# Kernel tuning notes

Measured on AMD Instinct MI355X. Metric: run time of the kernel, lower is better.

Reference implementation:

```python
import jax, jax.numpy as jnp
import numpy as np

B, T, LA, L = 4, 32, 32, 512
D, H, C = 2048, 16, 128
KV_DIM = 2048
K = T * LA  # total kv tokens per batch element
EPS = 1e-5


def _ln(x):
    m = jnp.mean(x, axis=-1, keepdims=True)
    v = jnp.var(x, axis=-1, keepdims=True)
    return (x - m) * jax.lax.rsqrt(v + EPS)


def setup_inputs() -> dict:
    key = jax.random.key(0)
    ks = jax.random.split(key, 10)
    s = 1.0 / np.sqrt(D)
    sk = 1.0 / np.sqrt(KV_DIM)
    return {
        "x": jax.random.normal(ks[0], (B, T, LA, KV_DIM), jnp.float32),
        "latents": jax.random.normal(ks[1], (B, L, D), jnp.float32),
        "t_emb": jax.random.normal(ks[2], (B, 3, D), jnp.float32) * 0.02,
        "q_lens": jnp.full((B,), L, dtype=jnp.int32),
        "k_lens": jax.random.randint(ks[3], (B,), K // 2, K + 1).astype(jnp.int32),
        "ln_kv_w": jnp.ones((KV_DIM,), jnp.float32),
        "ln_kv_b": jnp.zeros((KV_DIM,), jnp.float32),
        "ssg": jax.random.normal(ks[4], (1, 3, D), jnp.float32) * s,  # shift_scale_gate param (adaLN=True)
        "Wq": jax.random.normal(ks[5], (D, D), jnp.float32) * s,
        "bq": jnp.zeros((D,), jnp.float32),
        "Wkv": jax.random.normal(ks[6], (KV_DIM, 2 * D), jnp.float32) * sk,
        "bkv": jnp.zeros((2 * D,), jnp.float32),
        "Wo": jax.random.normal(ks[7], (D, D), jnp.float32) * s,
        "bo": jnp.zeros((D,), jnp.float32),
    }


def reference(x, latents, t_emb, q_lens, k_lens, ln_kv_w, ln_kv_b, ssg,
              Wq, bq, Wkv, bkv, Wo, bo):
    # norm_kv (affine LayerNorm over kv_dim)
    xk = _ln(x) * ln_kv_w + ln_kv_b  # (B,T,LA,KV_DIM)
    # AdaLN modulate: shift/scale/gate from t_emb + learned shift_scale_gate
    mod = t_emb + ssg  # (B,3,D)
    shift, scale, gate = mod[:, 0:1], mod[:, 1:2], mod[:, 2:3]  # (B,1,D)
    norm_q = _ln(latents)  # norm_q has no affine when adaLN=True
    lat = norm_q * (1.0 + scale) + shift
    # projections
    q = (lat @ Wq + bq).reshape(B, L, H, C)
    kv = (xk.reshape(B, K, KV_DIM) @ Wkv + bkv)  # (B,K,2D)
    k, v = kv[..., :D], kv[..., D:]
    k = k.reshape(B, K, H, C)
    v = v.reshape(B, K, H, C)
    # varlen attention == per-batch masked attention (keys beyond k_lens masked)
    scores = jnp.einsum("blhc,bkhc->bhlk", q, k) / np.sqrt(C)
    kmask = jnp.arange(K)[None, :] < k_lens[:, None]  # (B,K)
    scores = jnp.where(kmask[:, None, None, :], scores, jnp.finfo(scores.dtype).min)
    attn = jax.nn.softmax(scores, axis=-1)
    out = jnp.einsum("bhlk,bkhc->blhc", attn, v).reshape(B, L, D)
    # queries beyond q_lens are invalid -> zero them (varlen packing semantics)
    qmask = (jnp.arange(L)[None, :] < q_lens[:, None])[..., None]  # (B,L,1)
    out = out * qmask
    return (out @ Wo + bo) * gate
```

## Files before the change

### kernel.cpp

```cpp
#include <hip/hip_runtime.h>

typedef unsigned short u16;
typedef short bf16x8 __attribute__((ext_vector_type(8)));
typedef float f32x4 __attribute__((ext_vector_type(4)));

#define MFMA_BF16(a, b, c) __builtin_amdgcn_mfma_f32_16x16x32_bf16((a), (b), (c), 0, 0, 0)
#define ATT_SCALE 0.08838834764831845f

__device__ __forceinline__ u16 f2bf(float f) {
  union { float f; unsigned int u; } cv;
  cv.f = f;
  unsigned int u = cv.u + 0x7fffu + ((cv.u >> 16) & 1u);
  return (u16)(u >> 16);
}

__global__ __launch_bounds__(256) void ln_fused_kernel(
    const float* __restrict__ x, const float* __restrict__ w,
    const float* __restrict__ b, const float* __restrict__ latents,
    const float* __restrict__ t_emb, const float* __restrict__ ssg,
    u16* __restrict__ xk_out, u16* __restrict__ lat_out)
{
  const int blk = blockIdx.x;
  const bool is_x = blk < 4096;
  const int row = is_x ? blk : blk - 4096;
  const int tid = threadIdx.x;
  const float* src = is_x ? (x + (size_t)row * 2048) : (latents + (size_t)row * 2048);
  const float4* xr = (const float4*)src;
  float4 v0 = xr[tid];
  float4 v1 = xr[tid + 256];
  float sum = v0.x + v0.y + v0.z + v0.w + v1.x + v1.y + v1.z + v1.w;
  float sq  = v0.x*v0.x + v0.y*v0.y + v0.z*v0.z + v0.w*v0.w
            + v1.x*v1.x + v1.y*v1.y + v1.z*v1.z + v1.w*v1.w;
  #pragma unroll
  for (int off = 32; off > 0; off >>= 1) {
    sum += __shfl_xor(sum, off);
    sq  += __shfl_xor(sq, off);
  }
  __shared__ float red[8];
  if ((tid & 63) == 0) { red[tid >> 6] = sum; red[(tid >> 6) + 4] = sq; }
  __syncthreads();
  sum = red[0] + red[1] + red[2] + red[3];
  sq  = red[4] + red[5] + red[6] + red[7];
  const float mean = sum * (1.0f / 2048.0f);
  const float var  = sq * (1.0f / 2048.0f) - mean * mean;
  const float rstd = rsqrtf(var + 1e-5f);
  if (is_x) {
    const float4* w4 = (const float4*)w;
    const float4* b4 = (const float4*)b;
    ushort4* orow = (ushort4*)(xk_out + (size_t)row * 2048);
    #pragma unroll
    for (int j = 0; j < 2; ++j) {
      const int idx = tid + j * 256;
      const float4 v = j ? v1 : v0;
      const float4 ww = w4[idx];
      const float4 bb = b4[idx];
      ushort4 o;
      o.x = f2bf((v.x - mean) * rstd * ww.x + bb.x);
      o.y = f2bf((v.y - mean) * rstd * ww.y + bb.y);
      o.z = f2bf((v.z - mean) * rstd * ww.z + bb.z);
      o.w = f2bf((v.w - mean) * rstd * ww.w + bb.w);
      orow[idx] = o;
    }
  } else {
    const int bidx = row >> 9;
    const float4* te = (const float4*)(t_emb + (size_t)bidx * 3 * 2048);
    const float4* sg = (const float4*)ssg;
    ushort4* orow = (ushort4*)(lat_out + (size_t)row * 2048);
    #pragma unroll
    for (int j = 0; j < 2; ++j) {
      const int idx = tid + j * 256;
      const float4 v = j ? v1 : v0;
      const float4 t0 = te[idx];
      const float4 t1 = te[512 + idx];
      const float4 s0 = sg[idx];
      const float4 s1 = sg[512 + idx];
      ushort4 o;
      o.x = f2bf(((v.x - mean) * rstd) * (1.0f + t1.x + s1.x) + (t0.x + s0.x));
      o.y = f2bf(((v.y - mean) * rstd) * (1.0f + t1.y + s1.y) + (t0.y + s0.y));
      o.z = f2bf(((v.z - mean) * rstd) * (1.0f + t1.z + s1.z) + (t0.z + s0.z));
      o.w = f2bf(((v.w - mean) * rstd) * (1.0f + t1.w + s1.w) + (t0.w + s0.w));
      orow[idx] = o;
    }
  }
}

__global__ __launch_bounds__(256) void transpose_all_kernel(
    const float* __restrict__ Wq, const float* __restrict__ Wo,
    const float* __restrict__ Wkv,
    u16* __restrict__ WqT, u16* __restrict__ WoT, u16* __restrict__ WkvT)
{
  __shared__ float tile[32][33];
  int t = blockIdx.x;
  const float* in;
  u16* outp;
  int C, cx, ry;
  if (t < 4096)       { in = Wq;  outp = WqT;  C = 2048; cx = t & 63;  ry = t >> 6; }
  else if (t < 8192)  { t -= 4096; in = Wo;  outp = WoT;  C = 2048; cx = t & 63;  ry = t >> 6; }
  else                { t -= 8192; in = Wkv; outp = WkvT; C = 4096; cx = t & 127; ry = t >> 7; }
  const int R = 2048;
  const int c0 = cx * 32;
  const int r0 = ry * 32;
  const int tx = threadIdx.x & 31;
  const int ty = threadIdx.x >> 5;
  #pragma unroll
  for (int i = 0; i < 4; ++i)
    tile[ty + i * 8][tx] = in[(size_t)(r0 + ty + i * 8) * C + c0 + tx];
  __syncthreads();
  #pragma unroll
  for (int i = 0; i < 4; ++i)
    outp[(size_t)(c0 + ty + i * 8) * R + r0 + tx] = f2bf(tile[tx][ty + i * 8]);
}

template<int BM, int MODE>
__global__ __launch_bounds__(256) void gemm_bf16_kernel(
    const u16* __restrict__ A, const u16* __restrict__ BT,
    int Kd,
    const float* __restrict__ bias,
    u16* __restrict__ out_q, u16* __restrict__ out_k, u16* __restrict__ out_vT,
    float* __restrict__ out_f,
    const float* __restrict__ t_emb, const float* __restrict__ ssg)
{
  constexpr int TI = BM / 32;
  __shared__ u16 As[2][BM][40];
  __shared__ u16 Bs[2][128][40];
  const int tid  = threadIdx.x;
  const int lane = tid & 63;
  const int wv   = tid >> 6;
  const int wm   = wv & 1, wn = wv >> 1;
  const int quad = lane >> 4, lq = lane & 15;
  const int m0 = blockIdx.y * BM, n0 = blockIdx.x * 128;

  f32x4 acc[TI][4];
  #pragma unroll
  for (int i = 0; i < TI; ++i)
    #pragma unroll
    for (int j = 0; j < 4; ++j)
      acc[i][j] = (f32x4){0.f, 0.f, 0.f, 0.f};

  const int rB  = tid >> 1;
  const int hfB = (tid & 1) * 16;
  const u16* gB = BT + (size_t)(n0 + rB) * Kd + hfB;
  const int rA  = (BM == 128) ? (tid >> 1) : (tid >> 2);
  const int hA  = (BM == 128) ? 0 : ((tid >> 1) & 1);
  const int hfA = (tid & 1) * 16;
  const u16* gA = A + (size_t)(m0 + rA) * Kd + hA * 32 + hfA;

  for (int k0 = 0; k0 < Kd; k0 += 64) {
    uint4 a00, a01, a10, a11;
    a00 = *(const uint4*)(gA + k0);
    a01 = *(const uint4*)(gA + k0 + 8);
    if (BM == 128) {
      a10 = *(const uint4*)(gA + k0 + 32);
      a11 = *(const uint4*)(gA + k0 + 40);
    }
    const uint4 b00 = *(const uint4*)(gB + k0);
    const uint4 b01 = *(const uint4*)(gB + k0 + 8);
    const uint4 b10 = *(const uint4*)(gB + k0 + 32);
    const uint4 b11 = *(const uint4*)(gB + k0 + 40);
    __syncthreads();
    *(uint4*)&As[hA][rA][hfA]     = a00;
    *(uint4*)&As[hA][rA][hfA + 8] = a01;
    if (BM == 128) {
      *(uint4*)&As[1][rA][hfA]     = a10;
      *(uint4*)&As[1][rA][hfA + 8] = a11;
    }
    *(uint4*)&Bs[0][rB][hfB]     = b00;
    *(uint4*)&Bs[0][rB][hfB + 8] = b01;
    *(uint4*)&Bs[1][rB][hfB]     = b10;
    *(uint4*)&Bs[1][rB][hfB + 8] = b11;
    __syncthreads();
    #pragma unroll
    for (int kk = 0; kk < 2; ++kk) {
      bf16x8 av[TI], bv[4];
      #pragma unroll
      for (int i = 0; i < TI; ++i)
        av[i] = *(const bf16x8*)&As[kk][wm * (BM / 2) + i * 16 + lq][quad * 8];
      #pragma unroll
      for (int j = 0; j < 4; ++j)
        bv[j] = *(const bf16x8*)&Bs[kk][wn * 64 + j * 16 + lq][quad * 8];
      #pragma unroll
      for (int i = 0; i < TI; ++i)
        #pragma unroll
        for (int j = 0; j < 4; ++j)
          acc[i][j] = MFMA_BF16(av[i], bv[j], acc[i][j]);
    }
  }

  #pragma unroll
  for (int i = 0; i < TI; ++i) {
    const int mlb = m0 + wm * (BM / 2) + i * 16 + quad * 4;
    #pragma unroll
    for (int j = 0; j < 4; ++j) {
      const int n = n0 + wn * 64 + j * 16 + lq;
      const float bs = bias[n];
      if (MODE == 0) {
        const int h = n >> 7, c = n & 127;
        #pragma unroll
        for (int rr = 0; rr < 4; ++rr) {
          const int m = mlb + rr;
          const int bb = m >> 9, l = m & 511;
          out_q[((size_t)(bb * 16 + h) * 512 + l) * 128 + c] =
              f2bf((acc[i][j][rr] + bs) * ATT_SCALE);
        }
      } else if (MODE == 1) {
        if (n < 2048) {
          const int h = n >> 7, c = n & 127;
          #pragma unroll
          for (int rr = 0; rr < 4; ++rr) {
            const int m = mlb + rr;
            const int bb = m >> 10, kk = m & 1023;
            out_k[((size_t)(bb * 16 + h) * 1024 + kk) * 128 + c] = f2bf(acc[i][j][rr] + bs);
          }
        } else {
          const int n2 = n - 2048;
          const int h = n2 >> 7, c = n2 & 127;
          #pragma unroll
          for (int rr = 0; rr < 4; ++rr) {
            const int m = mlb + rr;
            const int bb = m >> 10, kk = m & 1023;
            out_vT[((size_t)(bb * 16 + h) * 128 + c) * 1024 + kk] = f2bf(acc[i][j][rr] + bs);
          }
        }
      } else {
        #pragma unroll
        for (int rr = 0; rr < 4; ++rr) {
          const int m = mlb + rr;
          const int bb = m >> 9;
          const float g = t_emb[((size_t)bb * 3 + 2) * 2048 + n] + ssg[2 * 2048 + n];
          out_f[(size_t)m * 2048 + n] = (acc[i][j][rr] + bs) * g;
        }
      }
    }
  }
}

__global__ __launch_bounds__(256) void attn_kernel(
    const u16* __restrict__ qb, const u16* __restrict__ kb,
    const u16* __restrict__ vT, const int* __restrict__ k_lens,
    const int* __restrict__ q_lens, u16* __restrict__ ao)
{
  __shared__ u16 Ks[64][132];
  __shared__ u16 Vs[128][68];
  __shared__ u16 Ps[64][68];
  const int tid  = threadIdx.x;
  const int w    = tid >> 6;
  const int lane = tid & 63;
  const int quad = lane >> 4, lq = lane & 15;
  const int bh = blockIdx.y;
  const int b  = bh >> 4;
  const int l0 = blockIdx.x * 64;
  const int kl = k_lens[b];
  const int ql = q_lens[b];

  bf16x8 qf[4];
  {
    const u16* qp = qb + ((size_t)bh * 512 + l0 + w * 16 + lq) * 128 + quad * 8;
    #pragma unroll
    for (int ks = 0; ks < 4; ++ks)
      qf[ks] = *(const bf16x8*)(qp + ks * 32);
  }

  const int krow = tid >> 4;
  const int kcol = tid & 15;
  const u16* kg = kb + ((size_t)bh * 1024 + krow) * 128 + kcol * 8;
  const int vrow = tid >> 3;
  const int vcol = tid & 7;
  const u16* vg = vT + (size_t)bh * 128 * 1024 + (size_t)vrow * 1024 + vcol * 8;

  f32x4 o[8];
  #pragma unroll
  for (int j = 0; j < 8; ++j) o[j] = (f32x4){0.f, 0.f, 0.f, 0.f};
  float mrun[4], lrun[4];
  #pragma unroll
  for (int rr = 0; rr < 4; ++rr) { mrun[rr] = -__builtin_inff(); lrun[rr] = 0.f; }

  const int nkt = (kl + 63) >> 6;
  for (int kt = 0; kt < nkt; ++kt) {
    const int k0 = kt * 64;
    uint4 kd[4], vd[4];
    #pragma unroll
    for (int p = 0; p < 4; ++p)
      kd[p] = *(const uint4*)(kg + (size_t)(k0 + p * 16) * 128);
    #pragma unroll
    for (int p = 0; p < 4; ++p)
      vd[p] = *(const uint4*)(vg + (size_t)p * 32 * 1024 + k0);
    __syncthreads();
    #pragma unroll
    for (int p = 0; p < 4; ++p)
      *(uint4*)&Ks[krow + p * 16][kcol * 8] = kd[p];
    #pragma unroll
    for (int p = 0; p < 4; ++p)
      *(uint4*)&Vs[vrow + p * 32][vcol * 8] = vd[p];
    __syncthreads();

    f32x4 s[4];
    #pragma unroll
    for (int ct = 0; ct < 4; ++ct) {
      s[ct] = (f32x4){0.f, 0.f, 0.f, 0.f};
      #pragma unroll
      for (int ks = 0; ks < 4; ++ks) {
        const bf16x8 kf = *(const bf16x8*)&Ks[ct * 16 + lq][ks * 32 + quad * 8];
        s[ct] = MFMA_BF16(qf[ks], kf, s[ct]);
      }
    }
    #pragma unroll
    for (int ct = 0; ct < 4; ++ct) {
      const bool valid = (k0 + ct * 16 + lq) < kl;
      #pragma unroll
      for (int rr = 0; rr < 4; ++rr)
        s[ct][rr] = valid ? s[ct][rr] : -__builtin_inff();
    }
    float mnew[4], alpha[4], rs[4];
    #pragma unroll
    for (int rr = 0; rr < 4; ++rr) {
      float tm = fmaxf(fmaxf(s[0][rr], s[1][rr]), fmaxf(s[2][rr], s[3][rr]));
      tm = fmaxf(tm, __shfl_xor(tm, 1));
      tm = fmaxf(tm, __shfl_xor(tm, 2));
      tm = fmaxf(tm, __shfl_xor(tm, 4));
      tm = fmaxf(tm, __shfl_xor(tm, 8));
      const float mn = fmaxf(mrun[rr], tm);
      alpha[rr] = __expf(mrun[rr] - mn);
      mrun[rr] = mn;
      mnew[rr] = mn;
      rs[rr] = 0.f;
    }
    #pragma unroll
    for (int ct = 0; ct < 4; ++ct)
      #pragma unroll
      for (int rr = 0; rr < 4; ++rr) {
        const float p = __expf(s[ct][rr] - mnew[rr]);
        s[ct][rr] = p;
        rs[rr] += p;
      }
    #pragma unroll
    for (int rr = 0; rr < 4; ++rr) {
      float t = rs[rr];
      t += __shfl_xor(t, 1);
      t += __shfl_xor(t, 2);
      t += __shfl_xor(t, 4);
      t += __shfl_xor(t, 8);
      lrun[rr] = lrun[rr] * alpha[rr] + t;
    }
    #pragma unroll
    for (int j = 0; j < 8; ++j)
      #pragma unroll
      for (int rr = 0; rr < 4; ++rr)
        o[j][rr] *= alpha[rr];

    #pragma unroll
    for (int ct = 0; ct < 4; ++ct)
      #pragma unroll
      for (int rr = 0; rr < 4; ++rr)
        Ps[w * 16 + quad * 4 + rr][ct * 16 + lq] = f2bf(s[ct][rr]);

    bf16x8 pf[2];
    pf[0] = *(const bf16x8*)&Ps[w * 16 + lq][quad * 8];
    pf[1] = *(const bf16x8*)&Ps[w * 16 + lq][32 + quad * 8];

    #pragma unroll
    for (int j = 0; j < 8; ++j) {
      #pragma unroll
      for (int kk = 0; kk < 2; ++kk) {
        const bf16x8 vf = *(const bf16x8*)&Vs[j * 16 + lq][kk * 32 + quad * 8];
        o[j] = MFMA_BF16(pf[kk], vf, o[j]);
      }
    }
  }

  const int h = bh & 15;
  #pragma unroll
  for (int rr = 0; rr < 4; ++rr) {
    const int row = l0 + w * 16 + quad * 4 + rr;
    const float inv = (row < ql) ? (1.0f / lrun[rr]) : 0.0f;
    u16* op = ao + ((size_t)b * 512 + row) * 2048 + h * 128 + lq;
    #pragma unroll
    for (int j = 0; j < 8; ++j)
      op[j * 16] = f2bf(o[j][rr] * inv);
  }
}

extern "C" void kernel_launch(void* const* d_in, const int* in_sizes, int n_in,
                              void* d_out, int out_size, void* d_ws, size_t ws_size,
                              hipStream_t stream) {
  (void)in_sizes; (void)n_in; (void)out_size; (void)ws_size;
  const float* x       = (const float*)d_in[0];
  const float* latents = (const float*)d_in[1];
  const float* t_emb   = (const float*)d_in[2];
  const int*   q_lens  = (const int*)d_in[3];
  const int*   k_lens  = (const int*)d_in[4];
  const float* ln_w    = (const float*)d_in[5];
  const float* ln_b    = (const float*)d_in[6];
  const float* ssg     = (const float*)d_in[7];
  const float* Wq      = (const float*)d_in[8];
  const float* bq      = (const float*)d_in[9];
  const float* Wkv     = (const float*)d_in[10];
  const float* bkv     = (const float*)d_in[11];
  const float* Wo      = (const float*)d_in[12];
  const float* bo      = (const float*)d_in[13];
  float* out = (float*)d_out;

  u16* ws = (u16*)d_ws;
  const size_t MEG = (size_t)1 << 20;
  u16* WqT  = ws;
  u16* WoT  = ws + 4  * MEG;
  u16* WkvT = ws + 8  * MEG;
  u16* xk   = ws + 16 * MEG;
  u16* lat  = ws + 24 * MEG;
  u16* qb   = ws + 28 * MEG;
  u16* kbuf = ws + 32 * MEG;
  u16* vTb  = ws + 40 * MEG;
  u16* aob  = ws + 48 * MEG;

  ln_fused_kernel<<<dim3(6144), dim3(256), 0, stream>>>(
      x, ln_w, ln_b, latents, t_emb, ssg, xk, lat);

  transpose_all_kernel<<<dim3(16384), dim3(256), 0, stream>>>(
      Wq, Wo, Wkv, WqT, WoT, WkvT);

  gemm_bf16_kernel<64, 0><<<dim3(16, 32), dim3(256), 0, stream>>>(
      lat, WqT, 2048, bq, qb, nullptr, nullptr, nullptr, nullptr, nullptr);
  gemm_bf16_kernel<128, 1><<<dim3(32, 32), dim3(256), 0, stream>>>(
      xk, WkvT, 2048, bkv, nullptr, kbuf, vTb, nullptr, nullptr, nullptr);

  attn_kernel<<<dim3(8, 64), dim3(256), 0, stream>>>(qb, kbuf, vTb, k_lens, q_lens, aob);

  gemm_bf16_kernel<64, 2><<<dim3(16, 32), dim3(256), 0, stream>>>(
      aob, WoT, 2048, bo, nullptr, nullptr, nullptr, out, t_emb, ssg);
}
```

Baseline: 432.0 us.

## Merge prep kernels, fuse Q and KV GEMMs, and prefetch next K-tile

Combines the LayerNorm and weight-transpose launches into one prep kernel, and merges the Q projection and KV projection into a single grouped GEMM launch with 128-row tiles for both. The GEMM main loop now issues the global loads for the next K-slice before running the MFMAs on the current one, a register-level software pipeline. The aim is to cut launch gaps and tail underutilisation and to overlap memory latency with compute. In exchange it uses more registers, the Q GEMM moves to larger tiles, and the mode is now picked at runtime inside the kernel.

```diff
diff --git a/kernel.cpp b/kernel.cpp
--- a/kernel.cpp
+++ b/kernel.cpp
@@ -14,113 +14,113 @@
   return (u16)(u >> 16);
 }
 
-__global__ __launch_bounds__(256) void ln_fused_kernel(
-    const float* __restrict__ x, const float* __restrict__ w,
-    const float* __restrict__ b, const float* __restrict__ latents,
+__global__ __launch_bounds__(256) void prep_kernel(
+    const float* __restrict__ x, const float* __restrict__ ln_w,
+    const float* __restrict__ ln_b, const float* __restrict__ latents,
     const float* __restrict__ t_emb, const float* __restrict__ ssg,
-    u16* __restrict__ xk_out, u16* __restrict__ lat_out)
-{
-  const int blk = blockIdx.x;
-  const bool is_x = blk < 4096;
-  const int row = is_x ? blk : blk - 4096;
-  const int tid = threadIdx.x;
-  const float* src = is_x ? (x + (size_t)row * 2048) : (latents + (size_t)row * 2048);
-  const float4* xr = (const float4*)src;
-  float4 v0 = xr[tid];
-  float4 v1 = xr[tid + 256];
-  float sum = v0.x + v0.y + v0.z + v0.w + v1.x + v1.y + v1.z + v1.w;
-  float sq  = v0.x*v0.x + v0.y*v0.y + v0.z*v0.z + v0.w*v0.w
-            + v1.x*v1.x + v1.y*v1.y + v1.z*v1.z + v1.w*v1.w;
-  #pragma unroll
-  for (int off = 32; off > 0; off >>= 1) {
-    sum += __shfl_xor(sum, off);
-    sq  += __shfl_xor(sq, off);
-  }
-  __shared__ float red[8];
-  if ((tid & 63) == 0) { red[tid >> 6] = sum; red[(tid >> 6) + 4] = sq; }
-  __syncthreads();
-  sum = red[0] + red[1] + red[2] + red[3];
-  sq  = red[4] + red[5] + red[6] + red[7];
-  const float mean = sum * (1.0f / 2048.0f);
-  const float var  = sq * (1.0f / 2048.0f) - mean * mean;
-  const float rstd = rsqrtf(var + 1e-5f);
-  if (is_x) {
-    const float4* w4 = (const float4*)w;
-    const float4* b4 = (const float4*)b;
-    ushort4* orow = (ushort4*)(xk_out + (size_t)row * 2048);
-    #pragma unroll
-    for (int j = 0; j < 2; ++j) {
-      const int idx = tid + j * 256;
-      const float4 v = j ? v1 : v0;
-      const float4 ww = w4[idx];
-      const float4 bb = b4[idx];
-      ushort4 o;
-      o.x = f2bf((v.x - mean) * rstd * ww.x + bb.x);
-      o.y = f2bf((v.y - mean) * rstd * ww.y + bb.y);
-      o.z = f2bf((v.z - mean) * rstd * ww.z + bb.z);
-      o.w = f2bf((v.w - mean) * rstd * ww.w + bb.w);
-      orow[idx] = o;
-    }
-  } else {
-    const int bidx = row >> 9;
-    const float4* te = (const float4*)(t_emb + (size_t)bidx * 3 * 2048);
-    const float4* sg = (const float4*)ssg;
-    ushort4* orow = (ushort4*)(lat_out + (size_t)row * 2048);
-    #pragma unroll
-    for (int j = 0; j < 2; ++j) {
-      const int idx = tid + j * 256;
-      const float4 v = j ? v1 : v0;
-      const float4 t0 = te[idx];
-      const float4 t1 = te[512 + idx];
-      const float4 s0 = sg[idx];
-      const float4 s1 = sg[512 + idx];
-      ushort4 o;
-      o.x = f2bf(((v.x - mean) * rstd) * (1.0f + t1.x + s1.x) + (t0.x + s0.x));
-      o.y = f2bf(((v.y - mean) * rstd) * (1.0f + t1.y + s1.y) + (t0.y + s0.y));
-      o.z = f2bf(((v.z - mean) * rstd) * (1.0f + t1.z + s1.z) + (t0.z + s0.z));
-      o.w = f2bf(((v.w - mean) * rstd) * (1.0f + t1.w + s1.w) + (t0.w + s0.w));
-      orow[idx] = o;
-    }
-  }
-}
-
-__global__ __launch_bounds__(256) void transpose_all_kernel(
     const float* __restrict__ Wq, const float* __restrict__ Wo,
     const float* __restrict__ Wkv,
+    u16* __restrict__ xk_out, u16* __restrict__ lat_out,
     u16* __restrict__ WqT, u16* __restrict__ WoT, u16* __restrict__ WkvT)
 {
-  __shared__ float tile[32][33];
-  int t = blockIdx.x;
-  const float* in;
-  u16* outp;
-  int C, cx, ry;
-  if (t < 4096)       { in = Wq;  outp = WqT;  C = 2048; cx = t & 63;  ry = t >> 6; }
-  else if (t < 8192)  { t -= 4096; in = Wo;  outp = WoT;  C = 2048; cx = t & 63;  ry = t >> 6; }
-  else                { t -= 8192; in = Wkv; outp = WkvT; C = 4096; cx = t & 127; ry = t >> 7; }
-  const int R = 2048;
-  const int c0 = cx * 32;
-  const int r0 = ry * 32;
-  const int tx = threadIdx.x & 31;
-  const int ty = threadIdx.x >> 5;
-  #pragma unroll
-  for (int i = 0; i < 4; ++i)
-    tile[ty + i * 8][tx] = in[(size_t)(r0 + ty + i * 8) * C + c0 + tx];
-  __syncthreads();
-  #pragma unroll
-  for (int i = 0; i < 4; ++i)
-    outp[(size_t)(c0 + ty + i * 8) * R + r0 + tx] = f2bf(tile[tx][ty + i * 8]);
+  __shared__ float shmem[32 * 33];
+  const int blk = blockIdx.x;
+  const int tid = threadIdx.x;
+  if (blk < 6144) {
+    const bool is_x = blk < 4096;
+    const int row = is_x ? blk : blk - 4096;
+    const float* src = is_x ? (x + (size_t)row * 2048) : (latents + (size_t)row * 2048);
+    const float4* xr = (const float4*)src;
+    float4 v0 = xr[tid];
+    float4 v1 = xr[tid + 256];
+    float sum = v0.x + v0.y + v0.z + v0.w + v1.x + v1.y + v1.z + v1.w;
+    float sq  = v0.x*v0.x + v0.y*v0.y + v0.z*v0.z + v0.w*v0.w
+              + v1.x*v1.x + v1.y*v1.y + v1.z*v1.z + v1.w*v1.w;
+    #pragma unroll
+    for (int off = 32; off > 0; off >>= 1) {
+      sum += __shfl_xor(sum, off);
+      sq  += __shfl_xor(sq, off);
+    }
+    if ((tid & 63) == 0) { shmem[tid >> 6] = sum; shmem[(tid >> 6) + 4] = sq; }
+    __syncthreads();
+    sum = shmem[0] + shmem[1] + shmem[2] + shmem[3];
+    sq  = shmem[4] + shmem[5] + shmem[6] + shmem[7];
+    const float mean = sum * (1.0f / 2048.0f);
+    const float var  = sq * (1.0f / 2048.0f) - mean * mean;
+    const float rstd = rsqrtf(var + 1e-5f);
+    if (is_x) {
+      const float4* w4 = (const float4*)ln_w;
+      const float4* b4 = (const float4*)ln_b;
+      ushort4* orow = (ushort4*)(xk_out + (size_t)row * 2048);
+      #pragma unroll
+      for (int j = 0; j < 2; ++j) {
+        const int idx = tid + j * 256;
+        const float4 v = j ? v1 : v0;
+        const float4 ww = w4[idx];
+        const float4 bb = b4[idx];
+        ushort4 o;
+        o.x = f2bf((v.x - mean) * rstd * ww.x + bb.x);
+        o.y = f2bf((v.y - mean) * rstd * ww.y + bb.y);
+        o.z = f2bf((v.z - mean) * rstd * ww.z + bb.z);
+        o.w = f2bf((v.w - mean) * rstd * ww.w + bb.w);
+        orow[idx] = o;
+      }
+    } else {
+      const int bidx = row >> 9;
+      const float4* te = (const float4*)(t_emb + (size_t)bidx * 3 * 2048);
+      const float4* sg = (const float4*)ssg;
+      ushort4* orow = (ushort4*)(lat_out + (size_t)row * 2048);
+      #pragma unroll
+      for (int j = 0; j < 2; ++j) {
+        const int idx = tid + j * 256;
+        const float4 v = j ? v1 : v0;
+        const float4 t0 = te[idx];
+        const float4 t1 = te[512 + idx];
+        const float4 s0 = sg[idx];
+        const float4 s1 = sg[512 + idx];
+        ushort4 o;
+        o.x = f2bf(((v.x - mean) * rstd) * (1.0f + t1.x + s1.x) + (t0.x + s0.x));
+        o.y = f2bf(((v.y - mean) * rstd) * (1.0f + t1.y + s1.y) + (t0.y + s0.y));
+        o.z = f2bf(((v.z - mean) * rstd) * (1.0f + t1.z + s1.z) + (t0.z + s0.z));
+        o.w = f2bf(((v.w - mean) * rstd) * (1.0f + t1.w + s1.w) + (t0.w + s0.w));
+        orow[idx] = o;
+      }
+    }
+  } else {
+    int t = blk - 6144;
+    const float* in;
+    u16* outp;
+    int C, cx, ry;
+    if (t < 4096)      { in = Wq;  outp = WqT;  C = 2048; cx = t & 63;  ry = t >> 6; }
+    else if (t < 8192) { t -= 4096; in = Wo;  outp = WoT;  C = 2048; cx = t & 63;  ry = t >> 6; }
+    else               { t -= 8192; in = Wkv; outp = WkvT; C = 4096; cx = t & 127; ry = t >> 7; }
+    float (*tile)[33] = (float(*)[33])shmem;
+    const int R = 2048;
+    const int c0 = cx * 32;
+    const int r0 = ry * 32;
+    const int tx = tid & 31;
+    const int ty = tid >> 5;
+    #pragma unroll
+    for (int i = 0; i < 4; ++i)
+      tile[ty + i * 8][tx] = in[(size_t)(r0 + ty + i * 8) * C + c0 + tx];
+    __syncthreads();
+    #pragma unroll
+    for (int i = 0; i < 4; ++i)
+      outp[(size_t)(c0 + ty + i * 8) * R + r0 + tx] = f2bf(tile[tx][ty + i * 8]);
+  }
 }
 
-template<int BM, int MODE>
-__global__ __launch_bounds__(256) void gemm_bf16_kernel(
-    const u16* __restrict__ A, const u16* __restrict__ BT,
-    int Kd,
-    const float* __restrict__ bias,
+template<int BM, int TMPL>
+__global__ __launch_bounds__(256) void gemm_kernel(
+    const u16* __restrict__ A0, const u16* __restrict__ BT0,
+    const u16* __restrict__ A1, const u16* __restrict__ BT1,
+    const float* __restrict__ bias0, const float* __restrict__ bias1,
     u16* __restrict__ out_q, u16* __restrict__ out_k, u16* __restrict__ out_vT,
     float* __restrict__ out_f,
     const float* __restrict__ t_emb, const float* __restrict__ ssg)
 {
   constexpr int TI = BM / 32;
+  constexpr int Kd = 2048;
   __shared__ u16 As[2][BM][40];
   __shared__ u16 Bs[2][128][40];
   const int tid  = threadIdx.x;
@@ -128,7 +128,20 @@
   const int wv   = tid >> 6;
   const int wm   = wv & 1, wn = wv >> 1;
   const int quad = lane >> 4, lq = lane & 15;
-  const int m0 = blockIdx.y * BM, n0 = blockIdx.x * 128;
+
+  int mode, m0, n0;
+  const u16 *A, *BT;
+  const float* bias;
+  if (TMPL == 3) {
+    int t = blockIdx.x;
+    if (t < 256) { mode = 0; A = A0; BT = BT0; bias = bias0;
+                   m0 = (t >> 4) * 128; n0 = (t & 15) * 128; }
+    else { t -= 256; mode = 1; A = A1; BT = BT1; bias = bias1;
+           m0 = (t >> 5) * 128; n0 = (t & 31) * 128; }
+  } else {
+    mode = 2; A = A0; BT = BT0; bias = bias0;
+    m0 = blockIdx.y * BM; n0 = blockIdx.x * 128;
+  }
 
   f32x4 acc[TI][4];
   #pragma unroll
@@ -145,18 +158,19 @@
   const int hfA = (tid & 1) * 16;
   const u16* gA = A + (size_t)(m0 + rA) * Kd + hA * 32 + hfA;
 
+  uint4 a00, a01, a10, a11, b00, b01, b10, b11;
+  a00 = *(const uint4*)(gA);
+  a01 = *(const uint4*)(gA + 8);
+  if (BM == 128) {
+    a10 = *(const uint4*)(gA + 32);
+    a11 = *(const uint4*)(gA + 40);
+  }
+  b00 = *(const uint4*)(gB);
+  b01 = *(const uint4*)(gB + 8);
+  b10 = *(const uint4*)(gB + 32);
+  b11 = *(const uint4*)(gB + 40);
+
   for (int k0 = 0; k0 < Kd; k0 += 64) {
-    uint4 a00, a01, a10, a11;
-    a00 = *(const uint4*)(gA + k0);
-    a01 = *(const uint4*)(gA + k0 + 8);
-    if (BM == 128) {
-      a10 = *(const uint4*)(gA + k0 + 32);
-      a11 = *(const uint4*)(gA + k0 + 40);
-    }
-    const uint4 b00 = *(const uint4*)(gB + k0);
-    const uint4 b01 = *(const uint4*)(gB + k0 + 8);
-    const uint4 b10 = *(const uint4*)(gB + k0 + 32);
-    const uint4 b11 = *(const uint4*)(gB + k0 + 40);
     __syncthreads();
     *(uint4*)&As[hA][rA][hfA]     = a00;
     *(uint4*)&As[hA][rA][hfA + 8] = a01;
@@ -169,6 +183,19 @@
     *(uint4*)&Bs[1][rB][hfB]     = b10;
     *(uint4*)&Bs[1][rB][hfB + 8] = b11;
     __syncthreads();
+
+    const int kn = (k0 + 64 < Kd) ? k0 + 64 : 0;
+    a00 = *(const uint4*)(gA + kn);
+    a01 = *(const uint4*)(gA + kn + 8);
+    if (BM == 128) {
+      a10 = *(const uint4*)(gA + kn + 32);
+      a11 = *(const uint4*)(gA + kn + 40);
+    }
+    b00 = *(const uint4*)(gB + kn);
+    b01 = *(const uint4*)(gB + kn + 8);
+    b10 = *(const uint4*)(gB + kn + 32);
+    b11 = *(const uint4*)(gB + kn + 40);
+
     #pragma unroll
     for (int kk = 0; kk < 2; ++kk) {
       bf16x8 av[TI], bv[4];
@@ -193,7 +220,7 @@
     for (int j = 0; j < 4; ++j) {
       const int n = n0 + wn * 64 + j * 16 + lq;
       const float bs = bias[n];
-      if (MODE == 0) {
+      if (mode == 0) {
         const int h = n >> 7, c = n & 127;
         #pragma unroll
         for (int rr = 0; rr < 4; ++rr) {
@@ -202,7 +229,7 @@
           out_q[((size_t)(bb * 16 + h) * 512 + l) * 128 + c] =
               f2bf((acc[i][j][rr] + bs) * ATT_SCALE);
         }
-      } else if (MODE == 1) {
+      } else if (mode == 1) {
         if (n < 2048) {
           const int h = n >> 7, c = n & 127;
           #pragma unroll
@@ -411,19 +438,15 @@
   u16* vTb  = ws + 40 * MEG;
   u16* aob  = ws + 48 * MEG;
 
-  ln_fused_kernel<<<dim3(6144), dim3(256), 0, stream>>>(
-      x, ln_w, ln_b, latents, t_emb, ssg, xk, lat);
-
-  transpose_all_kernel<<<dim3(16384), dim3(256), 0, stream>>>(
-      Wq, Wo, Wkv, WqT, WoT, WkvT);
-
-  gemm_bf16_kernel<64, 0><<<dim3(16, 32), dim3(256), 0, stream>>>(
-      lat, WqT, 2048, bq, qb, nullptr, nullptr, nullptr, nullptr, nullptr);
-  gemm_bf16_kernel<128, 1><<<dim3(32, 32), dim3(256), 0, stream>>>(
-      xk, WkvT, 2048, bkv, nullptr, kbuf, vTb, nullptr, nullptr, nullptr);
+  prep_kernel<<<dim3(22528), dim3(256), 0, stream>>>(
+      x, ln_w, ln_b, latents, t_emb, ssg, Wq, Wo, Wkv,
+      xk, lat, WqT, WoT, WkvT);
+
+  gemm_kernel<128, 3><<<dim3(1280), dim3(256), 0, stream>>>(
+      lat, WqT, xk, WkvT, bq, bkv, qb, kbuf, vTb, nullptr, nullptr, nullptr);
 
   attn_kernel<<<dim3(8, 64), dim3(256), 0, stream>>>(qb, kbuf, vTb, k_lens, q_lens, aob);
 
-  gemm_bf16_kernel<64, 2><<<dim3(16, 32), dim3(256), 0, stream>>>(
-      aob, WoT, 2048, bo, nullptr, nullptr, nullptr, out, t_emb, ssg);
+  gemm_kernel<64, 2><<<dim3(16, 32), dim3(256), 0, stream>>>(
+      aob, WoT, nullptr, nullptr, bo, nullptr, nullptr, nullptr, nullptr, out, t_emb, ssg);
 }
```

Result: no change. 433.8 us (+0.4%).
